# Optimization experiments

Hardware: AMD Instinct MI355X
Metric: run time of the kernel (lower is better)

The kernel has to match this reference:

```python
import jax, jax.numpy as jnp
import numpy as np

N_QUBITS = 4

def _rx(theta):
    # RX(t) = [[cos t/2, -i sin t/2], [-i sin t/2, cos t/2]]; theta scalar or [B]
    c = jnp.cos(theta / 2).astype(jnp.complex64)
    s = (-1j * jnp.sin(theta / 2)).astype(jnp.complex64)
    return jnp.stack([jnp.stack([c, s], -1), jnp.stack([s, c], -1)], -2)

def _ry(theta):
    c = jnp.cos(theta / 2).astype(jnp.complex64)
    s = jnp.sin(theta / 2).astype(jnp.complex64)
    return jnp.stack([jnp.stack([c, -s], -1), jnp.stack([s, c], -1)], -2)

def _rz(theta):
    e0 = jnp.exp(-0.5j * theta).astype(jnp.complex64)
    e1 = jnp.exp(0.5j * theta).astype(jnp.complex64)
    z = jnp.zeros_like(e0)
    return jnp.stack([jnp.stack([e0, z], -1), jnp.stack([z, e1], -1)], -2)

def _apply_1q(psi, U, wire):
    # psi: [B,2,2,2,2]; U: [2,2] (shared) or [B,2,2] (per-batch angle)
    psi = jnp.moveaxis(psi, 1 + wire, -1)
    if U.ndim == 3:
        psi = jnp.einsum('bij,b...j->b...i', U, psi)
    else:
        psi = jnp.einsum('ij,b...j->b...i', U, psi)
    return jnp.moveaxis(psi, -1, 1 + wire)

def _cnot(psi, c, t):
    psi = jnp.moveaxis(psi, (1 + c, 1 + t), (-2, -1))
    psi = jnp.concatenate([psi[..., 0:1, :], psi[..., 1:2, ::-1]], axis=-2)
    return jnp.moveaxis(psi, (-2, -1), (1 + c, 1 + t))

def _measure_all_z(psi):
    p = psi.real ** 2 + psi.imag ** 2  # [B,2,2,2,2]
    outs = []
    for w in range(N_QUBITS):
        shape = [1] * (N_QUBITS + 1)
        shape[1 + w] = 2
        z = jnp.array([1.0, -1.0], dtype=p.dtype).reshape(shape)
        outs.append(jnp.sum(p * z, axis=tuple(range(1, N_QUBITS + 1))))
    return jnp.stack(outs, -1)  # [B,4]

def _qlayer(x, theta):
    # x: [B,4] encoding angles; theta: [4] trainable RX angles
    B = x.shape[0]
    psi = jnp.zeros((B, 2 ** N_QUBITS), jnp.complex64).at[:, 0].set(1.0)
    psi = psi.reshape((B,) + (2,) * N_QUBITS)
    # encoder: rx(w0), ry(w1), rz(w2), rx(w3)
    psi = _apply_1q(psi, _rx(x[:, 0]), 0)
    psi = _apply_1q(psi, _ry(x[:, 1]), 1)
    psi = _apply_1q(psi, _rz(x[:, 2]), 2)
    psi = _apply_1q(psi, _rx(x[:, 3]), 3)
    # trainable RX on each wire
    for w in range(N_QUBITS):
        psi = _apply_1q(psi, _rx(theta[w]), w)
    # CNOT ring 0->1,1->2,2->3,3->0
    for w in range(N_QUBITS):
        psi = _cnot(psi, w, (w + 1) % N_QUBITS)
    return _measure_all_z(psi)

def setup_inputs() -> dict:
    key = jax.random.key(0)
    ks = jax.random.split(key, 13)
    T, B, D, H, Q = 128, 2048, 128, 4, 4
    s = 1.0 / np.sqrt(D + H)
    inp = {
        'inputs': jax.random.normal(ks[0], (T, B, D), jnp.float32),
        'Wf': jax.random.uniform(ks[1], (Q, D + H), jnp.float32, -s, s),
        'bf': jax.random.uniform(ks[2], (Q,), jnp.float32, -s, s),
        'Wi': jax.random.uniform(ks[3], (Q, D + H), jnp.float32, -s, s),
        'bi': jax.random.uniform(ks[4], (Q,), jnp.float32, -s, s),
        'Wu': jax.random.uniform(ks[5], (Q, D + H), jnp.float32, -s, s),
        'bu': jax.random.uniform(ks[6], (Q,), jnp.float32, -s, s),
        'Wo': jax.random.uniform(ks[7], (Q, D + H), jnp.float32, -s, s),
        'bo': jax.random.uniform(ks[8], (Q,), jnp.float32, -s, s),
        'theta_f': jax.random.uniform(ks[9], (Q,), jnp.float32, 0.0, 2 * np.pi),
        'theta_i': jax.random.uniform(ks[10], (Q,), jnp.float32, 0.0, 2 * np.pi),
        'theta_u': jax.random.uniform(ks[11], (Q,), jnp.float32, 0.0, 2 * np.pi),
        'theta_o': jax.random.uniform(ks[12], (Q,), jnp.float32, 0.0, 2 * np.pi),
    }
    return inp

def reference(inputs, Wf, bf, Wi, bi, Wu, bu, Wo, bo, theta_f, theta_i, theta_u, theta_o):
    T, B, D = inputs.shape
    H = N_QUBITS  # hidden_dim == n_qubits (required by elementwise gate math)
    h0 = jnp.zeros((B, H), inputs.dtype)
    c0 = jnp.zeros((B, H), inputs.dtype)

    def step(carry, x):
        hx, cx = carry
        comb = jnp.concatenate([x, hx], axis=1)  # [B, D+H]
        f = jax.nn.sigmoid(_qlayer(comb @ Wf.T + bf, theta_f))
        i = jax.nn.sigmoid(_qlayer(comb @ Wi.T + bi, theta_i))
        g = jnp.tanh(_qlayer(comb @ Wu.T + bu, theta_u))
        o = jax.nn.sigmoid(_qlayer(comb @ Wo.T + bo, theta_o))
        cx = f * cx + i * g
        hx = o * jnp.tanh(cx)
        return (hx, cx), hx

    (hx, cx), stacked = jax.lax.scan(step, (h0, c0), inputs)
    return stacked, hx, cx
```

## Files before the change

### kernel.cpp

```cpp
#include <hip/hip_runtime.h>

__device__ __forceinline__ float fast_exp(float x) {
  return __builtin_amdgcn_exp2f(x * 1.4426950408889634f);
}
__device__ __forceinline__ float fast_rcp(float x) {
  return __builtin_amdgcn_rcpf(x);
}
__device__ __forceinline__ float fast_cos(float x) {
  return __builtin_amdgcn_cosf(__builtin_amdgcn_fractf(x * 0.15915494309189535f));
}
__device__ __forceinline__ float fast_sigmoid(float x) {
  return fast_rcp(1.0f + fast_exp(-x));
}
__device__ __forceinline__ float fast_tanh(float x) {
  return 1.0f - 2.0f * fast_rcp(1.0f + fast_exp(2.0f * x));
}
__device__ __forceinline__ float sigmoid_poly(float x) {
  float x2 = x * x;
  float p = fmaf(fmaf(fmaf(-2.1085373e-4f, x2, 2.0833334e-3f), x2,
                      -2.0833334e-2f), x2, 0.25f);
  return fmaf(x, p, 0.5f);
}
__device__ __forceinline__ float tanh_pade(float x) {
  float x2 = x * x;
  float num = x * fmaf(x2 + 105.f, x2, 945.f);
  float den = fmaf(fmaf(15.f, x2, 420.f), x2, 945.f);
  return num * fast_rcp(den);
}

template <int CTRL>
__device__ __forceinline__ float dppf(float v) {
  return __int_as_float(__builtin_amdgcn_update_dpp(
      0, __float_as_int(v), CTRL, 0xf, 0xf, true));
}
#define QP_XOR1 0xB1
#define QP_XOR2 0x4E
#define QP_XOR3 0x1B

__global__ __launch_bounds__(64) void qlstm_gemm(
    const float* __restrict__ x,
    const float* __restrict__ Wf, const float* __restrict__ bf,
    const float* __restrict__ Wi, const float* __restrict__ bi,
    const float* __restrict__ Wu, const float* __restrict__ bu,
    const float* __restrict__ Wo, const float* __restrict__ bo,
    const float* __restrict__ thf, const float* __restrict__ thi,
    const float* __restrict__ thu, const float* __restrict__ tho,
    float* __restrict__ Z, long long rows, int B, int D)
{
  __shared__ float tile[64][36];
  const long long base = (long long)blockIdx.x * 64;
  const int tid = threadIdx.x;
  const long long r = base + tid;
  const bool valid = r < rows;
  const int ldw = D + 4;
  const float* Ws[4] = {Wf, Wi, Wu, Wo};
  const float* bs[4] = {bf, bi, bu, bo};
  const float* ts[4] = {thf, thi, thu, tho};

  float acc[12];
#pragma unroll
  for (int g = 0; g < 4; ++g) {
    acc[g * 3 + 0] = bs[g][0] + ts[g][0];
    acc[g * 3 + 1] = bs[g][1];
    acc[g * 3 + 2] = bs[g][3] + ts[g][3];
  }

  const int nkc = D >> 5;
  for (int kc = 0; kc < nkc; ++kc) {
#pragma unroll
    for (int i = 0; i < 8; ++i) {
      int f = i * 64 + tid;
      int row = f >> 3, col = (f & 7) * 4;
      long long gr = base + row;
      if (gr < rows) {
        float4 v = *(const float4*)(x + gr * (long long)D + kc * 32 + col);
        *(float4*)&tile[row][col] = v;
      }
    }
    __syncthreads();
    if (valid) {
#pragma unroll
      for (int k = 0; k < 32; k += 4) {
        float4 xv = *(float4*)&tile[tid][k];
#pragma unroll
        for (int g = 0; g < 4; ++g) {
#pragma unroll
          for (int jj = 0; jj < 3; ++jj) {
            int row2 = (jj == 2) ? 3 : jj;
            const float* wp = Ws[g] + row2 * ldw + kc * 32 + k;
            acc[g * 3 + jj] += xv.x * wp[0] + xv.y * wp[1] + xv.z * wp[2] + xv.w * wp[3];
          }
        }
      }
    }
    __syncthreads();
  }

  if (valid) {
    long long t = r / B;
    int b = (int)(r - t * B);
    float4 s0 = make_float4(acc[0], acc[3], acc[6], acc[9]);
    float4 s1 = make_float4(acc[1], acc[4], acc[7], acc[10]);
    float4 s2 = make_float4(acc[2], acc[5], acc[8], acc[11]);
    *(float4*)(Z + ((t * 3 + 0) * (long long)B + b) * 4) = s0;
    *(float4*)(Z + ((t * 3 + 1) * (long long)B + b) * 4) = s1;
    *(float4*)(Z + ((t * 3 + 2) * (long long)B + b) * 4) = s2;
  }
}

__global__ __launch_bounds__(64) void qlstm_scan4(
    const float* __restrict__ Z,
    const float* __restrict__ Wf, const float* __restrict__ Wi,
    const float* __restrict__ Wu, const float* __restrict__ Wo,
    const float* __restrict__ thf, const float* __restrict__ thi,
    const float* __restrict__ thu, const float* __restrict__ tho,
    float* __restrict__ out, int T, int B, int D)
{
  const int gid = blockIdx.x * 64 + threadIdx.x;
  const int b = gid >> 2, q = gid & 3;
  if (b >= B) return;

  const float* Wg = (q == 0) ? Wf : (q == 1) ? Wi : (q == 2) ? Wu : Wo;
  const float* th = (q == 0) ? thf : (q == 1) ? thi : (q == 2) ? thu : tho;
  const int ldw = D + 4;
  const float ct1 = fast_cos(th[1]);
  const float m2c = fast_cos(th[2]);

  float wh[3][4];
#pragma unroll
  for (int jj = 0; jj < 3; ++jj) {
    int row = (jj == 2) ? 3 : jj;
#pragma unroll
    for (int d = 0; d < 4; ++d)
      wh[jj][d] = Wg[row * ldw + D + (q ^ d)];
  }
  const bool e0 = ((q & 1) == 0);
  const bool e1 = ((q & 2) == 0);

  float h = 0.f, c = 0.f;

  const float* Zg = Z + gid;
  const size_t tstr = (size_t)12 * B;
  const size_t pstr = (size_t)4 * B;
  float* hx  = out + (size_t)T * B * 4;
  float* cxp = hx + (size_t)B * 4;

  auto ld3 = [&](int t, float& z0, float& z1, float& z2) {
    const float* p = Zg + (size_t)t * tstr;
    z0 = p[0]; z1 = p[pstr]; z2 = p[2 * pstr];
  };

  auto step = [&](float z0, float z1, float z2, int t) {
    float h1 = dppf<QP_XOR1>(h);
    float h2 = dppf<QP_XOR2>(h);
    float h3 = dppf<QP_XOR3>(h);
    float a0 = fmaf(wh[0][0], h, fmaf(wh[0][1], h1, fmaf(wh[0][2], h2, fmaf(wh[0][3], h3, z0))));
    float a1 = fmaf(wh[1][0], h, fmaf(wh[1][1], h1, fmaf(wh[1][2], h2, fmaf(wh[1][3], h3, z1))));
    float a2 = fmaf(wh[2][0], h, fmaf(wh[2][1], h1, fmaf(wh[2][2], h2, fmaf(wh[2][3], h3, z2))));
    float m0 = fast_cos(a0);
    float m1 = ct1 * fast_cos(a1);
    float m3 = fast_cos(a2);
    float m01 = m0 * m1, m23 = m2c * m3;
    float g0 = m1 * m23;
    float g1 = m01;
    float g2 = m01 * m2c;
    float g3 = m01 * m23;
    float x0 = dppf<QP_XOR1>(g0);
    float x1 = dppf<QP_XOR1>(g1);
    float x2 = dppf<QP_XOR1>(g2);
    float x3 = dppf<QP_XOR1>(g3);
    float s0 = e0 ? g0 : x1;
    float s1 = e0 ? x0 : g1;
    float s2 = e0 ? g2 : x3;
    float s3 = e0 ? x2 : g3;
    float y0 = dppf<QP_XOR2>(s0);
    float y1 = dppf<QP_XOR2>(s1);
    float y2 = dppf<QP_XOR2>(s2);
    float y3 = dppf<QP_XOR2>(s3);
    float wf_ = e1 ? s0 : y2;
    float wi_ = e1 ? s1 : y3;
    float wu_ = e1 ? y0 : s2;
    float wo_ = e1 ? y1 : s3;
    float fg = sigmoid_poly(wf_);
    float ig = sigmoid_poly(wi_);
    float ug = tanh_pade(wu_);
    float og = sigmoid_poly(wo_);
    c = fmaf(fg, c, ig * ug);
    h = og * tanh_pade(c);
    out[(size_t)t * pstr + gid] = h;
  };

  float A0, A1, A2, B0, B1, B2, C0, C1, C2, D0, D1, D2;
  if (T > 0) ld3(0, A0, A1, A2);
  if (T > 1) ld3(1, B0, B1, B2);
  if (T > 2) ld3(2, C0, C1, C2);
  if (T > 3) ld3(3, D0, D1, D2);

  int T4 = T & ~3;
  for (int t = 0; t < T4; t += 4) {
    { float z0 = A0, z1 = A1, z2 = A2;
      if (t + 4 < T) ld3(t + 4, A0, A1, A2);
      step(z0, z1, z2, t); }
    { float z0 = B0, z1 = B1, z2 = B2;
      if (t + 5 < T) ld3(t + 5, B0, B1, B2);
      step(z0, z1, z2, t + 1); }
    { float z0 = C0, z1 = C1, z2 = C2;
      if (t + 6 < T) ld3(t + 6, C0, C1, C2);
      step(z0, z1, z2, t + 2); }
    { float z0 = D0, z1 = D1, z2 = D2;
      if (t + 7 < T) ld3(t + 7, D0, D1, D2);
      step(z0, z1, z2, t + 3); }
  }
  for (int t = T4; t < T; ++t) {
    float z0, z1, z2;
    ld3(t, z0, z1, z2);
    step(z0, z1, z2, t);
  }
  hx[gid]  = h;
  cxp[gid] = c;
}

struct GK {
  float wh[4][3][4];
  float ct1[4];
  float m2c[4];
};

__device__ __forceinline__ void load_gk(GK& K,
    const float* Wf, const float* Wi, const float* Wu, const float* Wo,
    const float* thf, const float* thi, const float* thu, const float* tho,
    int D)
{
  const float* Ws[4] = {Wf, Wi, Wu, Wo};
  const float* ts[4] = {thf, thi, thu, tho};
  const int ldw = D + 4;
#pragma unroll
  for (int g = 0; g < 4; ++g) {
#pragma unroll
    for (int jj = 0; jj < 3; ++jj) {
      int row = (jj == 2) ? 3 : jj;
#pragma unroll
      for (int qq = 0; qq < 4; ++qq)
        K.wh[g][jj][qq] = Ws[g][row * ldw + D + qq];
    }
    K.ct1[g] = fast_cos(ts[g][1]);
    K.m2c[g] = fast_cos(ts[g][2]);
  }
}

__device__ __forceinline__ void qlstm_step_sc(const float a[12], const GK& K,
                                              float h[4], float c[4])
{
  float gv[4][4];
#pragma unroll
  for (int g = 0; g < 4; ++g) {
    float m0 = fast_cos(a[g * 3 + 0]);
    float m1 = K.ct1[g] * fast_cos(a[g * 3 + 1]);
    float m3 = fast_cos(a[g * 3 + 2]);
    float m01 = m0 * m1;
    float m23 = K.m2c[g] * m3;
    gv[g][0] = m1 * m23;
    gv[g][1] = m01;
    gv[g][2] = m01 * K.m2c[g];
    gv[g][3] = m01 * m23;
  }
#pragma unroll
  for (int qq = 0; qq < 4; ++qq) {
    float fg = fast_sigmoid(gv[0][qq]);
    float ig = fast_sigmoid(gv[1][qq]);
    float ug = fast_tanh(gv[2][qq]);
    float og = fast_sigmoid(gv[3][qq]);
    c[qq] = fg * c[qq] + ig * ug;
    h[qq] = og * fast_tanh(c[qq]);
  }
}

__global__ __launch_bounds__(256) void qlstm_fused(
    const float* __restrict__ x,
    const float* __restrict__ Wf, const float* __restrict__ bf,
    const float* __restrict__ Wi, const float* __restrict__ bi,
    const float* __restrict__ Wu, const float* __restrict__ bu,
    const float* __restrict__ Wo, const float* __restrict__ bo,
    const float* __restrict__ thf, const float* __restrict__ thi,
    const float* __restrict__ thu, const float* __restrict__ tho,
    float* __restrict__ out, int T, int B, int D)
{
  int b = blockIdx.x * 256 + threadIdx.x;
  if (b >= B) return;
  GK K;
  load_gk(K, Wf, Wi, Wu, Wo, thf, thi, thu, tho, D);
  const float* Ws[4] = {Wf, Wi, Wu, Wo};
  const float* bs[4] = {bf, bi, bu, bo};
  const float* ts[4] = {thf, thi, thu, tho};
  const int ldw = D + 4;

  float base[12];
#pragma unroll
  for (int g = 0; g < 4; ++g) {
    base[g * 3 + 0] = bs[g][0] + ts[g][0];
    base[g * 3 + 1] = bs[g][1];
    base[g * 3 + 2] = bs[g][3] + ts[g][3];
  }

  float h[4] = {0.f, 0.f, 0.f, 0.f};
  float c[4] = {0.f, 0.f, 0.f, 0.f};
  float* hx  = out + (size_t)T * B * 4;
  float* cxp = hx + (size_t)B * 4;

  for (int t = 0; t < T; ++t) {
    float a[12];
#pragma unroll
    for (int j = 0; j < 12; ++j) a[j] = base[j];
    const float* xp = x + ((size_t)t * B + b) * D;
    for (int k = 0; k < D; k += 4) {
      float4 xv = *(const float4*)(xp + k);
#pragma unroll
      for (int g = 0; g < 4; ++g) {
        const float* W = Ws[g];
#pragma unroll
        for (int jj = 0; jj < 3; ++jj) {
          int row = (jj == 2) ? 3 : jj;
          const float* wp = W + row * ldw + k;
          a[g * 3 + jj] += xv.x * wp[0] + xv.y * wp[1] + xv.z * wp[2] + xv.w * wp[3];
        }
      }
    }
#pragma unroll
    for (int g = 0; g < 4; ++g) {
#pragma unroll
      for (int jj = 0; jj < 3; ++jj) {
        a[g * 3 + jj] += K.wh[g][jj][0] * h[0] + K.wh[g][jj][1] * h[1]
                       + K.wh[g][jj][2] * h[2] + K.wh[g][jj][3] * h[3];
      }
    }
    qlstm_step_sc(a, K, h, c);
    *(float4*)(out + ((size_t)t * B + b) * 4) = make_float4(h[0], h[1], h[2], h[3]);
  }
  *(float4*)(hx + (size_t)b * 4)  = make_float4(h[0], h[1], h[2], h[3]);
  *(float4*)(cxp + (size_t)b * 4) = make_float4(c[0], c[1], c[2], c[3]);
}

extern "C" void kernel_launch(void* const* d_in, const int* in_sizes, int n_in,
                              void* d_out, int out_size, void* d_ws, size_t ws_size,
                              hipStream_t stream)
{
  const float* x   = (const float*)d_in[0];
  const float* Wf  = (const float*)d_in[1];
  const float* bf  = (const float*)d_in[2];
  const float* Wi  = (const float*)d_in[3];
  const float* bi  = (const float*)d_in[4];
  const float* Wu  = (const float*)d_in[5];
  const float* bu  = (const float*)d_in[6];
  const float* Wo  = (const float*)d_in[7];
  const float* bo  = (const float*)d_in[8];
  const float* thf = (const float*)d_in[9];
  const float* thi = (const float*)d_in[10];
  const float* thu = (const float*)d_in[11];
  const float* tho = (const float*)d_in[12];

  int DH = in_sizes[1] / 4;
  int D  = DH - 4;
  long long TB = (long long)in_sizes[0] / D;
  int B = (int)(((long long)out_size - 4 * TB) / 8);
  int T = (int)(TB / B);

  size_t zbytes = (size_t)TB * 12 * sizeof(float);
  if (ws_size >= zbytes && (D & 31) == 0) {
    float* Z = (float*)d_ws;
    int gblocks = (int)((TB + 63) / 64);
    qlstm_gemm<<<gblocks, 64, 0, stream>>>(x, Wf, bf, Wi, bi, Wu, bu, Wo, bo,
                                           thf, thi, thu, tho, Z, TB, B, D);
    int sthreads = B * 4;
    qlstm_scan4<<<(sthreads + 63) / 64, 64, 0, stream>>>(Z, Wf, Wi, Wu, Wo,
                                                         thf, thi, thu, tho,
                                                         (float*)d_out, T, B, D);
  } else {
    qlstm_fused<<<(B + 255) / 256, 256, 0, stream>>>(x, Wf, bf, Wi, bi, Wu, bu, Wo, bo,
                                                     thf, thi, thu, tho,
                                                     (float*)d_out, T, B, D);
  }
}
```

Measured before the change: 69.54 us.

## Double-buffer GEMM input via direct global-to-LDS loads and deepen scan prefetch

The input-projection GEMM now uses global_load_lds to copy x tiles straight into a double-buffered, XOR-swizzled LDS array. It keeps two chunks in flight and waits with vmcnt counters instead of loading through registers and using two barriers per chunk. The scan kernel's register prefetch ring grows from 4 to 8 timesteps to hide more Z load latency on the serial recurrence. The changes add register pressure and depend on vmcnt ordering being correct. The barriers are removed, which is only safe because each lane appears to read rows its own wave wrote.

```diff
diff --git a/kernel.cpp b/kernel.cpp
--- a/kernel.cpp
+++ b/kernel.cpp
@@ -1,4 +1,5 @@
 #include <hip/hip_runtime.h>
+#include <stdint.h>
 
 __device__ __forceinline__ float fast_exp(float x) {
   return __builtin_amdgcn_exp2f(x * 1.4426950408889634f);
@@ -36,6 +37,15 @@
 #define QP_XOR1 0xB1
 #define QP_XOR2 0x4E
 #define QP_XOR3 0x1B
+
+__device__ __forceinline__ void gload_lds16(const float* gp, const float* lp) {
+  __builtin_amdgcn_global_load_lds(
+      reinterpret_cast<const uint32_t __attribute__((address_space(1)))*>(
+          reinterpret_cast<uintptr_t>(gp)),
+      reinterpret_cast<uint32_t __attribute__((address_space(3)))*>(
+          reinterpret_cast<uintptr_t>(lp)),
+      16, 0, 0);
+}
 
 __global__ __launch_bounds__(64) void qlstm_gemm(
     const float* __restrict__ x,
@@ -47,7 +57,7 @@
     const float* __restrict__ thu, const float* __restrict__ tho,
     float* __restrict__ Z, long long rows, int B, int D)
 {
-  __shared__ float tile[64][36];
+  __shared__ float buf[2][64][32];
   const long long base = (long long)blockIdx.x * 64;
   const int tid = threadIdx.x;
   const long long r = base + tid;
@@ -57,6 +67,10 @@
   const float* bs[4] = {bf, bi, bu, bo};
   const float* ts[4] = {thf, thi, thu, tho};
 
+  const int lgrp = tid >> 3;
+  const int lcol = tid & 7;
+  const int scol4 = lcol ^ lgrp;
+
   float acc[12];
 #pragma unroll
   for (int g = 0; g < 4; ++g) {
@@ -66,22 +80,32 @@
   }
 
   const int nkc = D >> 5;
+
+  auto issue = [&](int kc, int w) {
+#pragma unroll
+    for (int i = 0; i < 8; ++i) {
+      long long gr = base + i * 8 + lgrp;
+      if (gr >= rows) gr = rows - 1;
+      const float* gp = x + gr * (long long)D + kc * 32 + scol4 * 4;
+      gload_lds16(gp, &buf[w][i * 8][0]);
+    }
+  };
+
+  issue(0, 0);
+  if (nkc > 1) issue(1, 1);
+
   for (int kc = 0; kc < nkc; ++kc) {
-#pragma unroll
-    for (int i = 0; i < 8; ++i) {
-      int f = i * 64 + tid;
-      int row = f >> 3, col = (f & 7) * 4;
-      long long gr = base + row;
-      if (gr < rows) {
-        float4 v = *(const float4*)(x + gr * (long long)D + kc * 32 + col);
-        *(float4*)&tile[row][col] = v;
-      }
-    }
-    __syncthreads();
+    if (kc + 2 < nkc) {
+      asm volatile("s_waitcnt vmcnt(8)" ::: "memory");
+    } else {
+      asm volatile("s_waitcnt vmcnt(0)" ::: "memory");
+    }
     if (valid) {
-#pragma unroll
-      for (int k = 0; k < 32; k += 4) {
-        float4 xv = *(float4*)&tile[tid][k];
+      const float(*tb)[32] = buf[kc & 1];
+#pragma unroll
+      for (int k4 = 0; k4 < 8; ++k4) {
+        float4 xv = *(const float4*)&tb[tid][(k4 ^ lcol) * 4];
+        int k = k4 * 4;
 #pragma unroll
         for (int g = 0; g < 4; ++g) {
 #pragma unroll
@@ -93,7 +117,7 @@
         }
       }
     }
-    __syncthreads();
+    if (kc + 2 < nkc) issue(kc + 2, kc & 1);
   }
 
   if (valid) {
@@ -191,27 +215,44 @@
   };
 
   float A0, A1, A2, B0, B1, B2, C0, C1, C2, D0, D1, D2;
+  float E0, E1, E2, F0, F1, F2, G0, G1, G2, H0, H1, H2;
   if (T > 0) ld3(0, A0, A1, A2);
   if (T > 1) ld3(1, B0, B1, B2);
   if (T > 2) ld3(2, C0, C1, C2);
   if (T > 3) ld3(3, D0, D1, D2);
-
-  int T4 = T & ~3;
-  for (int t = 0; t < T4; t += 4) {
+  if (T > 4) ld3(4, E0, E1, E2);
+  if (T > 5) ld3(5, F0, F1, F2);
+  if (T > 6) ld3(6, G0, G1, G2);
+  if (T > 7) ld3(7, H0, H1, H2);
+
+  int T8 = T & ~7;
+  for (int t = 0; t < T8; t += 8) {
     { float z0 = A0, z1 = A1, z2 = A2;
-      if (t + 4 < T) ld3(t + 4, A0, A1, A2);
+      if (t + 8 < T) ld3(t + 8, A0, A1, A2);
       step(z0, z1, z2, t); }
     { float z0 = B0, z1 = B1, z2 = B2;
-      if (t + 5 < T) ld3(t + 5, B0, B1, B2);
+      if (t + 9 < T) ld3(t + 9, B0, B1, B2);
       step(z0, z1, z2, t + 1); }
     { float z0 = C0, z1 = C1, z2 = C2;
-      if (t + 6 < T) ld3(t + 6, C0, C1, C2);
+      if (t + 10 < T) ld3(t + 10, C0, C1, C2);
       step(z0, z1, z2, t + 2); }
     { float z0 = D0, z1 = D1, z2 = D2;
-      if (t + 7 < T) ld3(t + 7, D0, D1, D2);
+      if (t + 11 < T) ld3(t + 11, D0, D1, D2);
       step(z0, z1, z2, t + 3); }
-  }
-  for (int t = T4; t < T; ++t) {
+    { float z0 = E0, z1 = E1, z2 = E2;
+      if (t + 12 < T) ld3(t + 12, E0, E1, E2);
+      step(z0, z1, z2, t + 4); }
+    { float z0 = F0, z1 = F1, z2 = F2;
+      if (t + 13 < T) ld3(t + 13, F0, F1, F2);
+      step(z0, z1, z2, t + 5); }
+    { float z0 = G0, z1 = G1, z2 = G2;
+      if (t + 14 < T) ld3(t + 14, G0, G1, G2);
+      step(z0, z1, z2, t + 6); }
+    { float z0 = H0, z1 = H1, z2 = H2;
+      if (t + 15 < T) ld3(t + 15, H0, H1, H2);
+      step(z0, z1, z2, t + 7); }
+  }
+  for (int t = T8; t < T; ++t) {
     float z0, z1, z2;
     ld3(t, z0, z1, z2);
     step(z0, z1, z2, t);
```

After: 80.50 us. 15.8% more time.

## Pack per-gate Z pre-activations as padded float4 and deepen scan prefetch

Applied to the files above, without the earlier changes.

The GEMM kernel now writes its three pre-activation values per gate into one padded float4 per (row, gate), instead of three planar float4 arrays. The scan kernel can then fetch all three values for a step with a single 16-byte load. The scan prefetch depth also grows from 4 to 8 timesteps to hide more memory latency on the serial recurrence. In exchange, the workspace and write traffic grow by a third because of the padding, and more registers are held per thread.

```diff
diff --git a/kernel.cpp b/kernel.cpp
--- a/kernel.cpp
+++ b/kernel.cpp
@@ -1,4 +1,5 @@
 #include <hip/hip_runtime.h>
+#include <stdint.h>
 
 __device__ __forceinline__ float fast_exp(float x) {
   return __builtin_amdgcn_exp2f(x * 1.4426950408889634f);
@@ -97,14 +98,12 @@
   }
 
   if (valid) {
-    long long t = r / B;
-    int b = (int)(r - t * B);
-    float4 s0 = make_float4(acc[0], acc[3], acc[6], acc[9]);
-    float4 s1 = make_float4(acc[1], acc[4], acc[7], acc[10]);
-    float4 s2 = make_float4(acc[2], acc[5], acc[8], acc[11]);
-    *(float4*)(Z + ((t * 3 + 0) * (long long)B + b) * 4) = s0;
-    *(float4*)(Z + ((t * 3 + 1) * (long long)B + b) * 4) = s1;
-    *(float4*)(Z + ((t * 3 + 2) * (long long)B + b) * 4) = s2;
+    float* zp = Z + r * 16;
+#pragma unroll
+    for (int g = 0; g < 4; ++g) {
+      *(float4*)(zp + g * 4) =
+          make_float4(acc[g * 3 + 0], acc[g * 3 + 1], acc[g * 3 + 2], 0.f);
+    }
   }
 }
 
@@ -139,18 +138,18 @@
 
   float h = 0.f, c = 0.f;
 
-  const float* Zg = Z + gid;
-  const size_t tstr = (size_t)12 * B;
+  const float* Zg = Z + (size_t)gid * 4;
+  const size_t tstr = (size_t)16 * B;
   const size_t pstr = (size_t)4 * B;
   float* hx  = out + (size_t)T * B * 4;
   float* cxp = hx + (size_t)B * 4;
 
-  auto ld3 = [&](int t, float& z0, float& z1, float& z2) {
-    const float* p = Zg + (size_t)t * tstr;
-    z0 = p[0]; z1 = p[pstr]; z2 = p[2 * pstr];
+  auto ld1 = [&](int t) -> float4 {
+    return *(const float4*)(Zg + (size_t)t * tstr);
   };
 
-  auto step = [&](float z0, float z1, float z2, int t) {
+  auto step = [&](float4 zv, int t) {
+    float z0 = zv.x, z1 = zv.y, z2 = zv.z;
     float h1 = dppf<QP_XOR1>(h);
     float h2 = dppf<QP_XOR2>(h);
     float h3 = dppf<QP_XOR3>(h);
@@ -190,31 +189,29 @@
     out[(size_t)t * pstr + gid] = h;
   };
 
-  float A0, A1, A2, B0, B1, B2, C0, C1, C2, D0, D1, D2;
-  if (T > 0) ld3(0, A0, A1, A2);
-  if (T > 1) ld3(1, B0, B1, B2);
-  if (T > 2) ld3(2, C0, C1, C2);
-  if (T > 3) ld3(3, D0, D1, D2);
-
-  int T4 = T & ~3;
-  for (int t = 0; t < T4; t += 4) {
-    { float z0 = A0, z1 = A1, z2 = A2;
-      if (t + 4 < T) ld3(t + 4, A0, A1, A2);
-      step(z0, z1, z2, t); }
-    { float z0 = B0, z1 = B1, z2 = B2;
-      if (t + 5 < T) ld3(t + 5, B0, B1, B2);
-      step(z0, z1, z2, t + 1); }
-    { float z0 = C0, z1 = C1, z2 = C2;
-      if (t + 6 < T) ld3(t + 6, C0, C1, C2);
-      step(z0, z1, z2, t + 2); }
-    { float z0 = D0, z1 = D1, z2 = D2;
-      if (t + 7 < T) ld3(t + 7, D0, D1, D2);
-      step(z0, z1, z2, t + 3); }
-  }
-  for (int t = T4; t < T; ++t) {
-    float z0, z1, z2;
-    ld3(t, z0, z1, z2);
-    step(z0, z1, z2, t);
+  float4 A, Bv, C, Dv, E, F, G, H;
+  if (T > 0) A  = ld1(0);
+  if (T > 1) Bv = ld1(1);
+  if (T > 2) C  = ld1(2);
+  if (T > 3) Dv = ld1(3);
+  if (T > 4) E  = ld1(4);
+  if (T > 5) F  = ld1(5);
+  if (T > 6) G  = ld1(6);
+  if (T > 7) H  = ld1(7);
+
+  int T8 = T & ~7;
+  for (int t = 0; t < T8; t += 8) {
+    { float4 zv = A;  if (t + 8  < T) A  = ld1(t + 8);  step(zv, t);     }
+    { float4 zv = Bv; if (t + 9  < T) Bv = ld1(t + 9);  step(zv, t + 1); }
+    { float4 zv = C;  if (t + 10 < T) C  = ld1(t + 10); step(zv, t + 2); }
+    { float4 zv = Dv; if (t + 11 < T) Dv = ld1(t + 11); step(zv, t + 3); }
+    { float4 zv = E;  if (t + 12 < T) E  = ld1(t + 12); step(zv, t + 4); }
+    { float4 zv = F;  if (t + 13 < T) F  = ld1(t + 13); step(zv, t + 5); }
+    { float4 zv = G;  if (t + 14 < T) G  = ld1(t + 14); step(zv, t + 6); }
+    { float4 zv = H;  if (t + 15 < T) H  = ld1(t + 15); step(zv, t + 7); }
+  }
+  for (int t = T8; t < T; ++t) {
+    step(ld1(t), t);
   }
   hx[gid]  = h;
   cxp[gid] = c;
@@ -364,7 +361,7 @@
   int B = (int)(((long long)out_size - 4 * TB) / 8);
   int T = (int)(TB / B);
 
-  size_t zbytes = (size_t)TB * 12 * sizeof(float);
+  size_t zbytes = (size_t)TB * 16 * sizeof(float);
   if (ws_size >= zbytes && (D & 31) == 0) {
     float* Z = (float*)d_ws;
     int gblocks = (int)((TB + 63) / 64);
```

Result: no change. 70.50 us (+1.4%).
